# Optimization experiments

Hardware: AMD Instinct MI355X
Metric: run time of the kernel (lower is better)

## Reference

```python
import jax, jax.numpy as jnp
import numpy as np

B, N, DIN, DOUT, D, C = 64, 8192, 64, 64, 10, 4
NPC = N // C  # nodes per client


def setup_inputs() -> dict:
    key = jax.random.key(0)
    ks = jax.random.split(key, 6)
    x = jax.random.normal(ks[0], (B, N, DIN), dtype=jnp.float32)
    node_embeddings = jax.random.normal(ks[1], (N, D), dtype=jnp.float32)
    poly_coefficients = jax.random.normal(ks[2], (C, 1, 4), dtype=jnp.float32)  # unused in sprtrelu mode
    mask = jnp.ones((B, N, 1), dtype=jnp.float32)
    weights_pool = jax.random.normal(ks[3], (C, D, DIN, DOUT), dtype=jnp.float32)
    bias_pool = jax.random.normal(ks[4], (C, D, DOUT), dtype=jnp.float32)
    nodes_per = jnp.arange(N, dtype=jnp.int64 if jax.config.x64_enabled else jnp.int32).reshape(C, NPC)
    return {"x": x, "node_embeddings": node_embeddings, "poly_coefficients": poly_coefficients,
            "mask": mask, "weights_pool": weights_pool, "bias_pool": bias_pool, "nodes_per": nodes_per}


def reference(x, node_embeddings, poly_coefficients, mask, weights_pool, bias_pool, nodes_per):
    # active_mode='sprtrelu', inter_dropout=0.0 -> bernoulli mask is all ones,
    # so sum_EH is the sum of EH over ALL clients, identical for every client.
    c, n = nodes_per.shape
    b = x.shape[0]
    x = x * mask                                       # [B,N,Din]
    E = node_embeddings[nodes_per]                     # [C,n,D] client-wise gather
    xg = jnp.take(x, nodes_per.reshape(-1), axis=1).reshape(b, c, n, -1)  # [B,C,n,Din]
    tE = jax.nn.relu(E)                                # [C,n,D]
    # per-client EH_c = einsum('nd,bnc->bdc'); sum over clients (bernoulli all ones)
    sum_EH = jnp.einsum('cnd,bcni->bdi', tE, xg)       # [B,D,Din]
    # Z_c = H_c + transformed_E_c @ sum_EH
    Z = xg + jnp.einsum('cnd,bdi->bcni', tE, sum_EH)   # [B,C,n,Din]
    # dynamic per-node weights/bias from embeddings
    W = jnp.einsum('cnd,cdio->cnio', E, weights_pool)  # [C,n,Din,Dout]
    bb = jnp.einsum('cnd,cdo->cno', E, bias_pool)      # [C,n,Dout]
    out = jnp.einsum('bcni,cnio->bcno', Z, W) + bb     # [B,C,n,Dout]
    return out.reshape(b, c * n, -1)                   # concat over clients along node dim
```

## Files before the change

kernel.cpp:

```cpp
#include <hip/hip_runtime.h>
#include <hip/hip_bf16.h>


#define BB 64
#define NN 8192
#define DI 64
#define DO 64
#define DD 10
#define CC 4
#define NPC 2048

typedef __bf16 bf16;
typedef __bf16 bf16x8 __attribute__((ext_vector_type(8)));
typedef __bf16 bf16x4 __attribute__((ext_vector_type(4)));
typedef float f32x4 __attribute__((ext_vector_type(4)));

__global__ __launch_bounds__(256) void k_sumEH(
    const float* __restrict__ x, const float* __restrict__ emb,
    const float* __restrict__ mask, const int* __restrict__ np,
    float* __restrict__ sEH) {
  __shared__ int np_l[512];
  __shared__ float mask_l[512];
  __shared__ float tEm[512][DD];
  __shared__ __align__(16) float red[4][DD][64];

  const int b = blockIdx.x >> 4;
  const int chunk = blockIdx.x & 15;
  const int tid = threadIdx.x;
  const int lane = tid & 63;
  const int w = tid >> 6;

  for (int s = tid; s < 512; s += 256) {
    const int node = np[chunk * 512 + s];
    np_l[s] = node;
    mask_l[s] = mask[(size_t)b * NN + node];
  }
  __syncthreads();
  for (int s = tid; s < 2560; s += 256) {
    const int nl = s / 5, pr = s % 5;
    const float2 e = *(const float2*)(emb + (size_t)np_l[nl] * DD + pr * 2);
    const float m = mask_l[nl];
    tEm[nl][pr * 2] = fmaxf(e.x, 0.f) * m;
    tEm[nl][pr * 2 + 1] = fmaxf(e.y, 0.f) * m;
  }
  __syncthreads();

  const int qq = lane >> 4, r16 = lane & 15;
  const f32x4* x4 = (const f32x4*)(x + (size_t)b * NN * DI);
  f32x4 acc[DD];
#pragma unroll
  for (int d = 0; d < DD; ++d) acc[d] = (f32x4)0.f;

  const int wbase = w * 128;
#pragma unroll 4
  for (int g = 0; g < 32; ++g) {
    const int nl = wbase + g * 4 + qq;
    const int node = np_l[nl];
    const f32x4 xv = x4[(size_t)node * 16 + r16];
#pragma unroll
    for (int d = 0; d < DD; ++d) {
      acc[d] += xv * tEm[nl][d];
    }
  }

#pragma unroll
  for (int d = 0; d < DD; ++d) {
    f32x4 a = acc[d];
#pragma unroll
    for (int j = 0; j < 4; ++j) {
      float v = a[j];
      v += __shfl_xor(v, 16);
      v += __shfl_xor(v, 32);
      a[j] = v;
    }
    acc[d] = a;
  }
  if (qq == 0) {
#pragma unroll
    for (int d = 0; d < DD; ++d) *(f32x4*)&red[w][d][r16 * 4] = acc[d];
  }
  __syncthreads();

  for (int s = tid; s < DD * 64; s += 256) {
    const int d = s >> 6, i = s & 63;
    const float v = red[0][d][i] + red[1][d][i] + red[2][d][i] + red[3][d][i];
    atomicAdd(sEH + ((size_t)b * DD + d) * 64 + i, v);
  }
}

__global__ __launch_bounds__(256) void k_main(
    const float* __restrict__ x, const float* __restrict__ emb,
    const float* __restrict__ mask, const float* __restrict__ wp,
    const float* __restrict__ bp, const int* __restrict__ np,
    const float* __restrict__ sEH, float* __restrict__ out) {
  __shared__ float E_l[4][DD];
  __shared__ float tE_l[4][DD];
  __shared__ float bb_l[4][64];
  __shared__ float mask_l[64][4];
  __shared__ int node_l[4];
  __shared__ __align__(16) bf16 Wt[4][64][80];
  __shared__ __align__(16) bf16 Zl[16][4][80];

  const int tid = threadIdx.x;
  const int lane = tid & 63;
  const int w = tid >> 6;
  const int p0 = blockIdx.x * 4;
  const int c = p0 >> 11;

  if (tid < 4) node_l[tid] = np[p0 + tid];
  if (tid < 40) {
    const int g = tid / 10, d = tid % 10;
    const float e = emb[(size_t)np[p0 + g] * DD + d];
    E_l[g][d] = e;
    tE_l[g][d] = fmaxf(e, 0.f);
  }
  {
    const int bq = tid >> 2, g = tid & 3;
    mask_l[bq][g] = mask[(size_t)bq * NN + np[p0 + g]];
  }
  __syncthreads();

  {
    float acc = 0.f;
#pragma unroll
    for (int d = 0; d < DD; ++d)
      acc = fmaf(E_l[w][d], bp[((size_t)(c * DD + d)) * DO + lane], acc);
    bb_l[w][lane] = acc;
  }

  {
    f32x4 accW[16];
#pragma unroll
    for (int p = 0; p < 16; ++p) accW[p] = (f32x4)0.f;
#pragma unroll
    for (int d = 0; d < DD; ++d) {
      f32x4 ev;
      ev[0] = E_l[0][d]; ev[1] = E_l[1][d]; ev[2] = E_l[2][d]; ev[3] = E_l[3][d];
      const float* wrow = wp + ((size_t)(c * DD + d) * DI + w * 16) * DO + lane;
#pragma unroll
      for (int p = 0; p < 16; ++p) accW[p] += ev * wrow[(size_t)p * DO];
    }
#pragma unroll
    for (int g = 0; g < 4; ++g) {
      bf16x8 v0, v1;
#pragma unroll
      for (int p = 0; p < 8; ++p) { v0[p] = (bf16)accW[p][g]; v1[p] = (bf16)accW[p + 8][g]; }
      *(bf16x8*)&Wt[g][lane][w * 16] = v0;
      *(bf16x8*)&Wt[g][lane][w * 16 + 8] = v1;
    }
  }

  const int gq = lane >> 4, i4 = lane & 15;
  const f32x4* x4 = (const f32x4*)x;
  const f32x4* s4 = (const f32x4*)sEH;

  for (int chunk = 0; chunk < 4; ++chunk) {
#pragma unroll
    for (int bb4 = 0; bb4 < 4; ++bb4) {
      const int b_loc = w * 4 + bb4;
      const int b = chunk * 16 + b_loc;
      const int nd = node_l[gq];
      f32x4 z = x4[((size_t)b * NN + nd) * 16 + i4];
      z *= mask_l[b][gq];
      const f32x4* sb = s4 + (size_t)b * DD * 16 + i4;
#pragma unroll
      for (int d = 0; d < DD; ++d) z += sb[d * 16] * tE_l[gq][d];
      bf16x4 zb;
#pragma unroll
      for (int j = 0; j < 4; ++j) zb[j] = (bf16)z[j];
      *(bf16x4*)&Zl[b_loc][gq][i4 * 4] = zb;
    }
    __syncthreads();

    {
      const int g = w;
      const int q = lane >> 4, r16 = lane & 15;
      f32x4 acc[4];
#pragma unroll
      for (int nt = 0; nt < 4; ++nt) {
        const float bv = bb_l[g][nt * 16 + r16];
        acc[nt][0] = bv; acc[nt][1] = bv; acc[nt][2] = bv; acc[nt][3] = bv;
      }
#pragma unroll
      for (int kt = 0; kt < 2; ++kt) {
        const int k0 = kt * 32 + q * 8;
        const bf16x8 a = *(const bf16x8*)&Zl[r16][g][k0];
#pragma unroll
        for (int nt = 0; nt < 4; ++nt) {
          const bf16x8 bfr = *(const bf16x8*)&Wt[g][nt * 16 + r16][k0];
          acc[nt] = __builtin_amdgcn_mfma_f32_16x16x32_bf16(a, bfr, acc[nt], 0, 0, 0);
        }
      }
      const size_t pg = (size_t)(p0 + g);
#pragma unroll
      for (int nt = 0; nt < 4; ++nt) {
#pragma unroll
        for (int r = 0; r < 4; ++r) {
          const int bg = chunk * 16 + q * 4 + r;
          out[((size_t)bg * NN + pg) * DO + nt * 16 + r16] = acc[nt][r];
        }
      }
    }
    __syncthreads();
  }
}

extern "C" void kernel_launch(void* const* d_in, const int* in_sizes, int n_in,
                              void* d_out, int out_size, void* d_ws, size_t ws_size,
                              hipStream_t stream) {
  const float* x    = (const float*)d_in[0];
  const float* emb  = (const float*)d_in[1];
  const float* mask = (const float*)d_in[3];
  const float* wp   = (const float*)d_in[4];
  const float* bp   = (const float*)d_in[5];
  const int*   np   = (const int*)d_in[6];
  float* out = (float*)d_out;
  float* sEH = (float*)d_ws;

  hipMemsetAsync(sEH, 0, (size_t)BB * DD * 64 * sizeof(float), stream);
  k_sumEH<<<dim3(BB * 16), dim3(256), 0, stream>>>(x, emb, mask, np, sEH);
  k_main<<<dim3(NN / 4), dim3(256), 0, stream>>>(x, emb, mask, wp, bp, np, sEH, out);
}
```

Before: 437.6 us.

## Restructure main kernel to build Z fragments in registers, double-buffer sumEH loads

The main kernel now handles 8 nodes per 512-thread block. Each wave builds its MFMA A-fragments for Z directly in registers, which removes the Zl shared buffer and the two barriers per batch chunk. W fragments and bias are held in registers across chunks. The sumEH kernel software-pipelines its gathered x loads with explicit double buffering and reads tE with vectorised float2 loads. The cost is higher register pressure, and the x reads per lane now follow a different coalescing pattern.

```diff
diff --git a/kernel.cpp b/kernel.cpp
--- a/kernel.cpp
+++ b/kernel.cpp
@@ -4,24 +4,20 @@
 
 #define BB 64
 #define NN 8192
-#define DI 64
-#define DO 64
 #define DD 10
 #define CC 4
-#define NPC 2048
 
 typedef __bf16 bf16;
 typedef __bf16 bf16x8 __attribute__((ext_vector_type(8)));
-typedef __bf16 bf16x4 __attribute__((ext_vector_type(4)));
 typedef float f32x4 __attribute__((ext_vector_type(4)));
 
-__global__ __launch_bounds__(256) void k_sumEH(
+__global__ __launch_bounds__(256, 4) void k_sumEH(
     const float* __restrict__ x, const float* __restrict__ emb,
     const float* __restrict__ mask, const int* __restrict__ np,
     float* __restrict__ sEH) {
   __shared__ int np_l[512];
   __shared__ float mask_l[512];
-  __shared__ float tEm[512][DD];
+  __shared__ __align__(8) float tEm[512][DD];
   __shared__ __align__(16) float red[4][DD][64];
 
   const int b = blockIdx.x >> 4;
@@ -46,22 +42,54 @@
   __syncthreads();
 
   const int qq = lane >> 4, r16 = lane & 15;
-  const f32x4* x4 = (const f32x4*)(x + (size_t)b * NN * DI);
+  const f32x4* x4 = (const f32x4*)(x + (size_t)b * NN * 64);
   f32x4 acc[DD];
 #pragma unroll
   for (int d = 0; d < DD; ++d) acc[d] = (f32x4)0.f;
 
   const int wbase = w * 128;
-#pragma unroll 4
-  for (int g = 0; g < 32; ++g) {
-    const int nl = wbase + g * 4 + qq;
-    const int node = np_l[nl];
-    const f32x4 xv = x4[(size_t)node * 16 + r16];
-#pragma unroll
-    for (int d = 0; d < DD; ++d) {
-      acc[d] += xv * tEm[nl][d];
-    }
-  }
+
+  int idA[4], idB[4];
+  f32x4 xvA[4], xvB[4];
+
+#define LOAD_IDS(buf, s_)                                        \
+  _Pragma("unroll") for (int t = 0; t < 4; ++t)                  \
+      buf[t] = np_l[wbase + ((s_) * 4 + t) * 4 + qq];
+#define LOAD_X(bufx, bufi)                                       \
+  _Pragma("unroll") for (int t = 0; t < 4; ++t)                  \
+      bufx[t] = x4[(size_t)bufi[t] * 16 + r16];
+#define FMA_BATCH(bufx, s_)                                      \
+  _Pragma("unroll") for (int t = 0; t < 4; ++t) {                \
+    const int nl = wbase + ((s_) * 4 + t) * 4 + qq;              \
+    const float2 t01 = *(const float2*)&tEm[nl][0];              \
+    const float2 t23 = *(const float2*)&tEm[nl][2];              \
+    const float2 t45 = *(const float2*)&tEm[nl][4];              \
+    const float2 t67 = *(const float2*)&tEm[nl][6];              \
+    const float2 t89 = *(const float2*)&tEm[nl][8];              \
+    const f32x4 xv = bufx[t];                                    \
+    acc[0] += xv * t01.x; acc[1] += xv * t01.y;                  \
+    acc[2] += xv * t23.x; acc[3] += xv * t23.y;                  \
+    acc[4] += xv * t45.x; acc[5] += xv * t45.y;                  \
+    acc[6] += xv * t67.x; acc[7] += xv * t67.y;                  \
+    acc[8] += xv * t89.x; acc[9] += xv * t89.y;                  \
+  }
+
+  LOAD_IDS(idA, 0)
+  LOAD_X(xvA, idA)
+#pragma unroll
+  for (int ss = 0; ss < 4; ++ss) {
+    LOAD_IDS(idB, 2 * ss + 1)
+    LOAD_X(xvB, idB)
+    FMA_BATCH(xvA, 2 * ss)
+    if (ss < 3) {
+      LOAD_IDS(idA, 2 * ss + 2)
+      LOAD_X(xvA, idA)
+    }
+    FMA_BATCH(xvB, 2 * ss + 1)
+  }
+#undef LOAD_IDS
+#undef LOAD_X
+#undef FMA_BATCH
 
 #pragma unroll
   for (int d = 0; d < DD; ++d) {
@@ -88,120 +116,135 @@
   }
 }
 
-__global__ __launch_bounds__(256) void k_main(
+__global__ __launch_bounds__(512, 4) void k_main(
     const float* __restrict__ x, const float* __restrict__ emb,
     const float* __restrict__ mask, const float* __restrict__ wp,
     const float* __restrict__ bp, const int* __restrict__ np,
     const float* __restrict__ sEH, float* __restrict__ out) {
-  __shared__ float E_l[4][DD];
-  __shared__ float tE_l[4][DD];
-  __shared__ float bb_l[4][64];
-  __shared__ float mask_l[64][4];
-  __shared__ int node_l[4];
-  __shared__ __align__(16) bf16 Wt[4][64][80];
-  __shared__ __align__(16) bf16 Zl[16][4][80];
+  __shared__ float E_l[8][DD];
+  __shared__ float bb_l[8][64];
+  __shared__ float mask_l[64][8];
+  __shared__ __align__(16) bf16 Wt[8][64][72];
 
   const int tid = threadIdx.x;
   const int lane = tid & 63;
   const int w = tid >> 6;
-  const int p0 = blockIdx.x * 4;
+  const int p0 = blockIdx.x * 8;
   const int c = p0 >> 11;
 
-  if (tid < 4) node_l[tid] = np[p0 + tid];
-  if (tid < 40) {
+  {
+    const int bq = tid >> 3, g = tid & 7;
+    mask_l[bq][g] = mask[(size_t)bq * NN + np[p0 + g]];
+  }
+  if (tid < 80) {
     const int g = tid / 10, d = tid % 10;
-    const float e = emb[(size_t)np[p0 + g] * DD + d];
-    E_l[g][d] = e;
-    tE_l[g][d] = fmaxf(e, 0.f);
-  }
+    E_l[g][d] = emb[(size_t)np[p0 + g] * DD + d];
+  }
+  __syncthreads();
+
   {
-    const int bq = tid >> 2, g = tid & 3;
-    mask_l[bq][g] = mask[(size_t)bq * NN + np[p0 + g]];
-  }
-  __syncthreads();
-
-  {
-    float acc = 0.f;
+    f32x4 aLo[8], aHi[8];
+#pragma unroll
+    for (int p = 0; p < 8; ++p) { aLo[p] = (f32x4)0.f; aHi[p] = (f32x4)0.f; }
+#pragma unroll
+    for (int d = 0; d < DD; ++d) {
+      f32x4 eLo, eHi;
+      eLo[0] = E_l[0][d]; eLo[1] = E_l[1][d]; eLo[2] = E_l[2][d]; eLo[3] = E_l[3][d];
+      eHi[0] = E_l[4][d]; eHi[1] = E_l[5][d]; eHi[2] = E_l[6][d]; eHi[3] = E_l[7][d];
+      const float* base = wp + ((size_t)(c * DD + d) * 64 + w * 8) * 64 + lane;
+#pragma unroll
+      for (int p = 0; p < 8; ++p) {
+        const float v = base[(size_t)p * 64];
+        aLo[p] += eLo * v;
+        aHi[p] += eHi * v;
+      }
+    }
+#pragma unroll
+    for (int g = 0; g < 8; ++g) {
+      bf16x8 v;
+#pragma unroll
+      for (int p = 0; p < 8; ++p) v[p] = (bf16)((g < 4) ? aLo[p][g] : aHi[p][g - 4]);
+      *(bf16x8*)&Wt[g][lane][w * 8] = v;
+    }
+    float bacc = 0.f;
 #pragma unroll
     for (int d = 0; d < DD; ++d)
-      acc = fmaf(E_l[w][d], bp[((size_t)(c * DD + d)) * DO + lane], acc);
-    bb_l[w][lane] = acc;
-  }
-
-  {
-    f32x4 accW[16];
-#pragma unroll
-    for (int p = 0; p < 16; ++p) accW[p] = (f32x4)0.f;
-#pragma unroll
-    for (int d = 0; d < DD; ++d) {
-      f32x4 ev;
-      ev[0] = E_l[0][d]; ev[1] = E_l[1][d]; ev[2] = E_l[2][d]; ev[3] = E_l[3][d];
-      const float* wrow = wp + ((size_t)(c * DD + d) * DI + w * 16) * DO + lane;
-#pragma unroll
-      for (int p = 0; p < 16; ++p) accW[p] += ev * wrow[(size_t)p * DO];
-    }
-#pragma unroll
-    for (int g = 0; g < 4; ++g) {
-      bf16x8 v0, v1;
-#pragma unroll
-      for (int p = 0; p < 8; ++p) { v0[p] = (bf16)accW[p][g]; v1[p] = (bf16)accW[p + 8][g]; }
-      *(bf16x8*)&Wt[g][lane][w * 16] = v0;
-      *(bf16x8*)&Wt[g][lane][w * 16 + 8] = v1;
-    }
-  }
-
-  const int gq = lane >> 4, i4 = lane & 15;
+      bacc = fmaf(E_l[w][d], bp[((size_t)(c * DD + d)) * 64 + lane], bacc);
+    bb_l[w][lane] = bacc;
+  }
+  __syncthreads();
+
+  const int mynode = np[p0 + w];
+  const int q = lane >> 4, r16 = lane & 15;
+
+  bf16x8 wfrag[4][2];
+#pragma unroll
+  for (int nt = 0; nt < 4; ++nt)
+#pragma unroll
+    for (int kt = 0; kt < 2; ++kt)
+      wfrag[nt][kt] = *(const bf16x8*)&Wt[w][nt * 16 + r16][kt * 32 + q * 8];
+
+  float biasv[4];
+#pragma unroll
+  for (int nt = 0; nt < 4; ++nt) biasv[nt] = bb_l[w][nt * 16 + r16];
+
+  float tEr[DD];
+#pragma unroll
+  for (int d = 0; d < DD; ++d) tEr[d] = fmaxf(E_l[w][d], 0.f);
+
   const f32x4* x4 = (const f32x4*)x;
   const f32x4* s4 = (const f32x4*)sEH;
 
+#pragma unroll
   for (int chunk = 0; chunk < 4; ++chunk) {
-#pragma unroll
-    for (int bb4 = 0; bb4 < 4; ++bb4) {
-      const int b_loc = w * 4 + bb4;
-      const int b = chunk * 16 + b_loc;
-      const int nd = node_l[gq];
-      f32x4 z = x4[((size_t)b * NN + nd) * 16 + i4];
-      z *= mask_l[b][gq];
-      const f32x4* sb = s4 + (size_t)b * DD * 16 + i4;
-#pragma unroll
-      for (int d = 0; d < DD; ++d) z += sb[d * 16] * tE_l[gq][d];
-      bf16x4 zb;
-#pragma unroll
-      for (int j = 0; j < 4; ++j) zb[j] = (bf16)z[j];
-      *(bf16x4*)&Zl[b_loc][gq][i4 * 4] = zb;
-    }
-    __syncthreads();
-
-    {
-      const int g = w;
-      const int q = lane >> 4, r16 = lane & 15;
-      f32x4 acc[4];
-#pragma unroll
-      for (int nt = 0; nt < 4; ++nt) {
-        const float bv = bb_l[g][nt * 16 + r16];
-        acc[nt][0] = bv; acc[nt][1] = bv; acc[nt][2] = bv; acc[nt][3] = bv;
+    const int b = chunk * 16 + r16;
+    const float m = mask_l[b][w];
+    const size_t xrow = ((size_t)b * NN + mynode) * 16;
+    f32x4 z00 = x4[xrow + q * 2 + 0] * m;
+    f32x4 z01 = x4[xrow + q * 2 + 1] * m;
+    f32x4 z10 = x4[xrow + 8 + q * 2 + 0] * m;
+    f32x4 z11 = x4[xrow + 8 + q * 2 + 1] * m;
+    const f32x4* sb = s4 + (size_t)b * DD * 16 + q * 2;
+#pragma unroll
+    for (int d = 0; d < DD; ++d) {
+      const f32x4 s0 = sb[d * 16 + 0];
+      const f32x4 s1 = sb[d * 16 + 1];
+      const f32x4 s2 = sb[d * 16 + 8];
+      const f32x4 s3 = sb[d * 16 + 9];
+      const float t = tEr[d];
+      z00 += s0 * t;
+      z01 += s1 * t;
+      z10 += s2 * t;
+      z11 += s3 * t;
+    }
+    bf16x8 a0, a1;
+#pragma unroll
+    for (int j = 0; j < 4; ++j) {
+      a0[j] = (bf16)z00[j];
+      a0[4 + j] = (bf16)z01[j];
+      a1[j] = (bf16)z10[j];
+      a1[4 + j] = (bf16)z11[j];
+    }
+    f32x4 acc[4];
+#pragma unroll
+    for (int nt = 0; nt < 4; ++nt) {
+      acc[nt][0] = biasv[nt]; acc[nt][1] = biasv[nt];
+      acc[nt][2] = biasv[nt]; acc[nt][3] = biasv[nt];
+    }
+#pragma unroll
+    for (int nt = 0; nt < 4; ++nt) {
+      acc[nt] = __builtin_amdgcn_mfma_f32_16x16x32_bf16(a0, wfrag[nt][0], acc[nt], 0, 0, 0);
+      acc[nt] = __builtin_amdgcn_mfma_f32_16x16x32_bf16(a1, wfrag[nt][1], acc[nt], 0, 0, 0);
+    }
+    const size_t pg = (size_t)(p0 + w);
+#pragma unroll
+    for (int nt = 0; nt < 4; ++nt) {
+#pragma unroll
+      for (int r = 0; r < 4; ++r) {
+        const int bg = chunk * 16 + q * 4 + r;
+        out[((size_t)bg * NN + pg) * 64 + nt * 16 + r16] = acc[nt][r];
       }
-#pragma unroll
-      for (int kt = 0; kt < 2; ++kt) {
-        const int k0 = kt * 32 + q * 8;
-        const bf16x8 a = *(const bf16x8*)&Zl[r16][g][k0];
-#pragma unroll
-        for (int nt = 0; nt < 4; ++nt) {
-          const bf16x8 bfr = *(const bf16x8*)&Wt[g][nt * 16 + r16][k0];
-          acc[nt] = __builtin_amdgcn_mfma_f32_16x16x32_bf16(a, bfr, acc[nt], 0, 0, 0);
-        }
-      }
-      const size_t pg = (size_t)(p0 + g);
-#pragma unroll
-      for (int nt = 0; nt < 4; ++nt) {
-#pragma unroll
-        for (int r = 0; r < 4; ++r) {
-          const int bg = chunk * 16 + q * 4 + r;
-          out[((size_t)bg * NN + pg) * DO + nt * 16 + r16] = acc[nt][r];
-        }
-      }
-    }
-    __syncthreads();
+    }
   }
 }
 
@@ -219,5 +262,5 @@
 
   hipMemsetAsync(sEH, 0, (size_t)BB * DD * 64 * sizeof(float), stream);
   k_sumEH<<<dim3(BB * 16), dim3(256), 0, stream>>>(x, emb, mask, np, sEH);
-  k_main<<<dim3(NN / 4), dim3(256), 0, stream>>>(x, emb, mask, wp, bp, np, sEH, out);
+  k_main<<<dim3(NN / 8), dim3(512), 0, stream>>>(x, emb, mask, wp, bp, np, sEH, out);
 }
```

Result: faster. 426.8 us (-2.5%).
